# Kernel optimization log

Hardware: AMD Instinct MI355X
Metric: run time of the kernel (lower is better)

Reference implementation:

```python
import jax, jax.numpy as jnp
import numpy as np

N = 100000
E = 1600000
D_IN = 128
HID = 128
N_CLASSES = 40
NEG_SLOPE = 0.2  # PyG GATConv default
BN_EPS = 1e-5


def setup_inputs() -> dict:
    key = jax.random.key(0)
    ks = jax.random.split(key, 16)
    s = 0.1
    return {
        "x": jax.random.normal(ks[0], (N, D_IN), dtype=jnp.float32),
        "edge_index": jax.random.randint(ks[1], (2, E), 0, N, dtype=jnp.int64),
        # GAT layer 1 (in=D_IN, out=HID, heads=1)
        "W1": jax.random.normal(ks[2], (D_IN, HID), dtype=jnp.float32) * s,
        "a_src1": jax.random.normal(ks[3], (HID,), dtype=jnp.float32) * s,
        "a_dst1": jax.random.normal(ks[4], (HID,), dtype=jnp.float32) * s,
        "b1": jnp.zeros((HID,), dtype=jnp.float32),
        # GAT layer 2 (in=HID, out=HID, heads=1)
        "W2": jax.random.normal(ks[5], (HID, HID), dtype=jnp.float32) * s,
        "a_src2": jax.random.normal(ks[6], (HID,), dtype=jnp.float32) * s,
        "a_dst2": jax.random.normal(ks[7], (HID,), dtype=jnp.float32) * s,
        "b2": jnp.zeros((HID,), dtype=jnp.float32),
        # shared BatchNorm1d(HID) applied after every conv
        "gamma": jnp.ones((HID,), dtype=jnp.float32),
        "beta": jnp.zeros((HID,), dtype=jnp.float32),
        # output Linear(HID, N_CLASSES)
        "Wout": jax.random.normal(ks[8], (HID, N_CLASSES), dtype=jnp.float32) * s,
        "bout": jnp.zeros((N_CLASSES,), dtype=jnp.float32),
    }


def reference(x, edge_index, W1, a_src1, a_dst1, b1, W2, a_src2, a_dst2, b2,
              gamma, beta, Wout, bout):
    n = x.shape[0]
    loops = jnp.arange(n, dtype=edge_index.dtype)  # add_self_loops (GATConv default)
    src = jnp.concatenate([edge_index[0], loops])
    dst = jnp.concatenate([edge_index[1], loops])

    def gat_layer(h_in, W, a_s, a_d, b):
        h = h_in @ W                                   # [N, HID]
        e_src = h @ a_s                                # [N] per-node src score
        e_dst = h @ a_d                                # [N] per-node dst score
        e = jax.nn.leaky_relu(e_src[src] + e_dst[dst], NEG_SLOPE)  # [E+N]
        # segment softmax over incoming edges of each dst node
        m = jax.ops.segment_max(e, dst, num_segments=n)
        p = jnp.exp(e - m[dst])
        denom = jax.ops.segment_sum(p, dst, num_segments=n)
        alpha = p / denom[dst]
        out = jax.ops.segment_sum(alpha[:, None] * h[src], dst, num_segments=n)
        return out + b

    def bn_elu(z):
        mu = z.mean(axis=0)
        var = ((z - mu) ** 2).mean(axis=0)  # biased var (BN training mode)
        zh = (z - mu) / jnp.sqrt(var + BN_EPS) * gamma + beta
        return jax.nn.elu(zh)

    h = bn_elu(gat_layer(x, W1, a_src1, a_dst1, b1))
    h = bn_elu(gat_layer(h, W2, a_src2, a_dst2, b2))
    return h @ Wout + bout
```

## Files before the change

kernel.cpp:

```cpp
#include <hip/hip_runtime.h>

#define NNODES 100000
#define NEDGES 1600000
#define ET (NEDGES + NNODES)
#define NBUCK 782
#define NEG 0.2f
#define BNEPS 1e-5f
#define EPB 4096
#define NBLK_E ((ET + EPB - 1) / EPB)
#define CAP 4096

typedef __attribute__((ext_vector_type(8))) short short8;
typedef __attribute__((ext_vector_type(4))) float floatx4;
typedef __attribute__((ext_vector_type(2))) float floatx2;

__device__ __forceinline__ unsigned short f2b(float x) {
    unsigned int u = __float_as_uint(x);
    u += 0x7fff + ((u >> 16) & 1);
    return (unsigned short)(u >> 16);
}
__device__ __forceinline__ float b2f(unsigned short u) {
    return __uint_as_float(((unsigned int)u) << 16);
}
__device__ __forceinline__ float blo2f(unsigned int v) {
    return __uint_as_float(v << 16);
}
__device__ __forceinline__ float bhi2f(unsigned int v) {
    return __uint_as_float(v & 0xffff0000u);
}
__device__ __forceinline__ floatx2 u2f2(unsigned int v) {
    floatx2 r;
    r.x = __uint_as_float(v << 16);
    r.y = __uint_as_float(v & 0xffff0000u);
    return r;
}

__device__ __forceinline__ int edge_src(const int* ei, int e, int w64) {
    if (e >= NEDGES) return e - NEDGES;
    return w64 ? ei[2 * e] : ei[e];
}
__device__ __forceinline__ int edge_dst(const int* ei, int e, int w64) {
    if (e >= NEDGES) return e - NEDGES;
    return w64 ? ei[2 * (NEDGES + e)] : ei[NEDGES + e];
}

__global__ void k_prep(const float* __restrict__ W1, const float* __restrict__ W2,
                       unsigned short* __restrict__ WT1, unsigned short* __restrict__ WT2,
                       const int* ei, int* flag, int* bcur, float* bnstat) {
    int t = blockIdx.x * 256 + threadIdx.x;
    if (t < 800) bcur[t] = t * CAP;
    if (blockIdx.x == 4) {
        bnstat[threadIdx.x] = 0.f;
    } else if (blockIdx.x == 5) {
        bnstat[256 + threadIdx.x] = 0.f;
    }
    if (t == 1) {
        int is64 = 1;
        for (int j = 1; j < 16; j += 2)
            if (ei[j] != 0) is64 = 0;
        *flag = is64;
    }
    int k = t >> 7, n = t & 127;
    WT1[n * 128 + k] = f2b(W1[t]);
    WT2[n * 128 + k] = f2b(W2[t]);
}

__global__ __launch_bounds__(256) void k_bscatter(const int* __restrict__ ei,
                                                  const int* flag, int* bcur,
                                                  int* __restrict__ pairs) {
    __shared__ int lc[784];
    __shared__ int lbase[784];
    int t = threadIdx.x;
    for (int i = t; i < NBUCK; i += 256) lc[i] = 0;
    __syncthreads();
    int w64 = *flag;
    int base = blockIdx.x * EPB;
    for (int j = 0; j < EPB / 512; j++) {
        int e = base + j * 512 + t * 2;
        if (e + 1 < NEDGES) {
            int d0, d1;
            if (w64) {
                int4 dv = *(const int4*)&ei[2 * (NEDGES + e)];
                d0 = dv.x; d1 = dv.z;
            } else {
                int2 dv = *(const int2*)&ei[NEDGES + e];
                d0 = dv.x; d1 = dv.y;
            }
            atomicAdd(&lc[d0 >> 7], 1);
            atomicAdd(&lc[d1 >> 7], 1);
        } else {
            for (int k = 0; k < 2; k++) {
                int ee = e + k;
                if (ee < ET) atomicAdd(&lc[edge_dst(ei, ee, w64) >> 7], 1);
            }
        }
    }
    __syncthreads();
    for (int i = t; i < NBUCK; i += 256)
        if (lc[i]) lbase[i] = atomicAdd(&bcur[i], lc[i]);
    __syncthreads();
    for (int j = 0; j < EPB / 512; j++) {
        int e = base + j * 512 + t * 2;
        if (e + 1 < NEDGES) {
            int s0, s1, d0, d1;
            if (w64) {
                int4 sv = *(const int4*)&ei[2 * e];
                int4 dv = *(const int4*)&ei[2 * (NEDGES + e)];
                s0 = sv.x; s1 = sv.z; d0 = dv.x; d1 = dv.z;
            } else {
                int2 sv = *(const int2*)&ei[e];
                int2 dv = *(const int2*)&ei[NEDGES + e];
                s0 = sv.x; s1 = sv.y; d0 = dv.x; d1 = dv.y;
            }
            int p0 = atomicAdd(&lbase[d0 >> 7], 1);
            pairs[p0] = (s0 << 7) | (d0 & 127);
            int p1 = atomicAdd(&lbase[d1 >> 7], 1);
            pairs[p1] = (s1 << 7) | (d1 & 127);
        } else {
            for (int k = 0; k < 2; k++) {
                int ee = e + k;
                if (ee < ET) {
                    int src = edge_src(ei, ee, w64);
                    int dst = edge_dst(ei, ee, w64);
                    int pos = atomicAdd(&lbase[dst >> 7], 1);
                    pairs[pos] = (src << 7) | (dst & 127);
                }
            }
        }
    }
}

__global__ __launch_bounds__(256) void k_bsort(const int* __restrict__ pairs,
                                               const int* __restrict__ bcur,
                                               int2* __restrict__ rowse,
                                               int* __restrict__ srcs) {
    __shared__ int ncnt[128];
    __shared__ int nbase[128];
    __shared__ int sscan[128];
    int b = blockIdx.x, t = threadIdx.x;
    if (t < 128) ncnt[t] = 0;
    __syncthreads();
    int s0 = b * CAP, s1 = bcur[b];
    for (int i = s0 + t; i < s1; i += 256)
        atomicAdd(&ncnt[pairs[i] & 127], 1);
    __syncthreads();
    int v = (t < 128) ? ncnt[t] : 0;
    if (t < 128) sscan[t] = v;
    __syncthreads();
    for (int off = 1; off < 128; off <<= 1) {
        int add = (t < 128 && t >= off) ? sscan[t - off] : 0;
        __syncthreads();
        if (t < 128) sscan[t] += add;
        __syncthreads();
    }
    if (t < 128) {
        int excl = sscan[t] - v;
        nbase[t] = excl;
        int node = b * 128 + t;
        if (node < NNODES) rowse[node] = make_int2(s0 + excl, s0 + excl + v);
    }
    __syncthreads();
    if (t < 128) ncnt[t] = nbase[t];
    __syncthreads();
    for (int i = s0 + t; i < s1; i += 256) {
        int pr = pairs[i];
        int off = atomicAdd(&ncnt[pr & 127], 1);
        srcs[s0 + off] = ((unsigned int)pr) >> 7;
    }
}

template<bool BN>
__global__ __launch_bounds__(256) void k_gemm(const void* __restrict__ Ain,
        const unsigned short* __restrict__ WTg,
        const float* __restrict__ sums, const float* __restrict__ sqs,
        const float* __restrict__ gamma, const float* __restrict__ beta,
        const float* __restrict__ a_s, const float* __restrict__ a_d,
        float* __restrict__ es, float* __restrict__ ed,
        unsigned short* __restrict__ hB, int n) {
    __shared__ unsigned short lA[128][136];
    __shared__ unsigned short lW[128][136];
    __shared__ float las[128], lad[128];
    __shared__ float lsc[128], lsh[128];
    int t = threadIdx.x;
    int row0 = blockIdx.x * 128;
    if (t < 128) { las[t] = a_s[t]; lad[t] = a_d[t]; }
    if (BN && t < 128) {
        float mu = sums[t] * (1.f / NNODES);
        float var = fmaxf(sqs[t] * (1.f / NNODES) - mu * mu, 0.f);
        float s = gamma[t] * rsqrtf(var + BNEPS);
        lsc[t] = s;
        lsh[t] = beta[t] - mu * s;
    }

    const uint4* wt4 = (const uint4*)WTg;
#pragma unroll
    for (int j = 0; j < 8; j++) {
        int idx = t + j * 256;
        *(uint4*)&lW[idx >> 4][(idx & 15) * 8] = wt4[idx];
    }
    if (BN) __syncthreads();

    if (BN) {
        const uint4* Ab = (const uint4*)Ain;
#pragma unroll
        for (int j = 0; j < 8; j++) {
            int idx = t + j * 256;
            int r = idx >> 4, seg = idx & 15;
            uint4 v = make_uint4(0, 0, 0, 0);
            if (row0 + r < n) v = Ab[(size_t)(row0 + r) * 16 + seg];
            float f[8];
            f[0] = blo2f(v.x); f[1] = bhi2f(v.x);
            f[2] = blo2f(v.y); f[3] = bhi2f(v.y);
            f[4] = blo2f(v.z); f[5] = bhi2f(v.z);
            f[6] = blo2f(v.w); f[7] = bhi2f(v.w);
            unsigned short us[8];
#pragma unroll
            for (int k = 0; k < 8; k++) {
                int c = seg * 8 + k;
                float z = fmaf(f[k], lsc[c], lsh[c]);
                z = z > 0.f ? z : __expf(z) - 1.f;
                us[k] = f2b(z);
            }
            ushort4 u0, u1;
            u0.x = us[0]; u0.y = us[1]; u0.z = us[2]; u0.w = us[3];
            u1.x = us[4]; u1.y = us[5]; u1.z = us[6]; u1.w = us[7];
            *(ushort4*)&lA[r][seg * 8] = u0;
            *(ushort4*)&lA[r][seg * 8 + 4] = u1;
        }
    } else {
        const float* Af = (const float*)Ain;
#pragma unroll
        for (int j = 0; j < 16; j++) {
            int idx = t + j * 256;
            int r = idx >> 5, c4 = idx & 31;
            float4 v = make_float4(0.f, 0.f, 0.f, 0.f);
            if (row0 + r < n) v = ((const float4*)Af)[(size_t)(row0 + r) * 32 + c4];
            ushort4 u;
            u.x = f2b(v.x); u.y = f2b(v.y); u.z = f2b(v.z); u.w = f2b(v.w);
            *(ushort4*)&lA[r][c4 * 4] = u;
        }
    }
    __syncthreads();

    int w = t >> 6, lane = t & 63;
    int m = lane & 15, q = lane >> 4;
    int ar0 = w * 32 + m, ar1 = w * 32 + 16 + m;
    floatx4 acc0[8], acc1[8];
#pragma unroll
    for (int ct = 0; ct < 8; ct++) { acc0[ct] = (floatx4)0.0f; acc1[ct] = (floatx4)0.0f; }

#pragma unroll
    for (int kt = 0; kt < 4; kt++) {
        int kb = kt * 32 + q * 8;
        short8 af0 = *(const short8*)&lA[ar0][kb];
        short8 af1 = *(const short8*)&lA[ar1][kb];
#pragma unroll
        for (int ct = 0; ct < 8; ct++) {
            short8 bf = *(const short8*)&lW[ct * 16 + m][kb];
            acc0[ct] = __builtin_amdgcn_mfma_f32_16x16x32_bf16(af0, bf, acc0[ct], 0, 0, 0);
            acc1[ct] = __builtin_amdgcn_mfma_f32_16x16x32_bf16(af1, bf, acc1[ct], 0, 0, 0);
        }
    }

    __syncthreads();
#pragma unroll
    for (int ct = 0; ct < 8; ct++)
#pragma unroll
        for (int r = 0; r < 4; r++) {
            lA[w * 32 + q * 4 + r][ct * 16 + m] = f2b(acc0[ct][r]);
            lA[w * 32 + 16 + q * 4 + r][ct * 16 + m] = f2b(acc1[ct][r]);
        }
    __syncthreads();
#pragma unroll
    for (int j = 0; j < 8; j++) {
        int idx = t + j * 256;
        int r = idx >> 4, seg = idx & 15;
        int grow = row0 + r;
        if (grow < n) {
            uint4 v = *(const uint4*)&lA[r][seg * 8];
            ((uint4*)hB)[(size_t)grow * 16 + seg] = v;
        }
    }
    int r = t >> 1, q2 = t & 1;
    float s1 = 0.f, s2 = 0.f;
#pragma unroll
    for (int k = 0; k < 32; k++) {
        int c = q2 * 64 + 2 * k;
        unsigned int u = *(const unsigned int*)&lA[r][c];
        float va = blo2f(u), vb = bhi2f(u);
        s1 += va * las[c] + vb * las[c + 1];
        s2 += va * lad[c] + vb * lad[c + 1];
    }
    s1 += __shfl_xor(s1, 1, 64);
    s2 += __shfl_xor(s2, 1, 64);
    if (q2 == 0 && row0 + r < n) { es[row0 + r] = s1; ed[row0 + r] = s2; }
}

__global__ __launch_bounds__(256) void k_attn(const unsigned short* __restrict__ hB,
                                              const int* __restrict__ srcs,
                                              const int2* __restrict__ rowse,
                                              const float* __restrict__ es,
                                              const float* __restrict__ ed,
                                              const float* __restrict__ bias,
                                              unsigned short* __restrict__ haggB, int n) {
    __shared__ uint2 sp[8][32];
    int w = (blockIdx.x * 256 + threadIdx.x) >> 5;
    if (w >= n) return;
    int hw = threadIdx.x >> 5;
    int lane32 = threadIdx.x & 31;
    int g = lane32 >> 4, l16 = lane32 & 15;
    int2 se = rowse[w];
    int start = se.x, end = se.y;
    float edv = ed[w];
    const uint4* hp4 = (const uint4*)hB;
    floatx2 a0 = {0.f, 0.f}, a1 = {0.f, 0.f}, a2 = {0.f, 0.f}, a3 = {0.f, 0.f};
    float den = 0.f;

    for (int chunk = start; chunk < end; chunk += 32) {
        int i = chunk + lane32;
        int sv = 0; float pv = 0.f;
        if (i < end) {
            sv = srcs[i];
            float e = es[sv] + edv;
            e = e > 0.f ? e : NEG * e;
            pv = __expf(e);
            den += pv;
        }
        sp[hw][lane32] = make_uint2((unsigned)sv, __float_as_uint(pv));
        int cnt = min(32, end - chunk);
        for (int j = 0; j < cnt; j += 8) {
            uint2 e0 = sp[hw][j + g];
            uint2 e1 = sp[hw][j + 2 + g];
            uint2 e2 = sp[hw][j + 4 + g];
            uint2 e3 = sp[hw][j + 6 + g];
            uint4 h0 = hp4[e0.x * 16u + l16];
            uint4 h1 = hp4[e1.x * 16u + l16];
            uint4 h2 = hp4[e2.x * 16u + l16];
            uint4 h3 = hp4[e3.x * 16u + l16];
            float p0 = __uint_as_float(e0.y), p1 = __uint_as_float(e1.y);
            float p2 = __uint_as_float(e2.y), p3 = __uint_as_float(e3.y);
            floatx2 P0 = {p0, p0};
            a0 += P0 * u2f2(h0.x); a1 += P0 * u2f2(h0.y);
            a2 += P0 * u2f2(h0.z); a3 += P0 * u2f2(h0.w);
            floatx2 P1 = {p1, p1};
            a0 += P1 * u2f2(h1.x); a1 += P1 * u2f2(h1.y);
            a2 += P1 * u2f2(h1.z); a3 += P1 * u2f2(h1.w);
            floatx2 P2 = {p2, p2};
            a0 += P2 * u2f2(h2.x); a1 += P2 * u2f2(h2.y);
            a2 += P2 * u2f2(h2.z); a3 += P2 * u2f2(h2.w);
            floatx2 P3 = {p3, p3};
            a0 += P3 * u2f2(h3.x); a1 += P3 * u2f2(h3.y);
            a2 += P3 * u2f2(h3.z); a3 += P3 * u2f2(h3.w);
        }
    }
    den += __shfl_xor(den, 1, 64);  den += __shfl_xor(den, 2, 64);
    den += __shfl_xor(den, 4, 64);  den += __shfl_xor(den, 8, 64);
    den += __shfl_xor(den, 16, 64);
    a0.x += __shfl_xor(a0.x, 16, 64); a0.y += __shfl_xor(a0.y, 16, 64);
    a1.x += __shfl_xor(a1.x, 16, 64); a1.y += __shfl_xor(a1.y, 16, 64);
    a2.x += __shfl_xor(a2.x, 16, 64); a2.y += __shfl_xor(a2.y, 16, 64);
    a3.x += __shfl_xor(a3.x, 16, 64); a3.y += __shfl_xor(a3.y, 16, 64);
    if (g == 0) {
        float inv = 1.f / den;
        const float2* b2p = (const float2*)bias;
        float2 c0 = b2p[l16 * 4 + 0], c1 = b2p[l16 * 4 + 1];
        float2 c2 = b2p[l16 * 4 + 2], c3 = b2p[l16 * 4 + 3];
        uint4 o;
        o.x = (unsigned int)f2b(fmaf(a0.x, inv, c0.x)) |
              ((unsigned int)f2b(fmaf(a0.y, inv, c0.y)) << 16);
        o.y = (unsigned int)f2b(fmaf(a1.x, inv, c1.x)) |
              ((unsigned int)f2b(fmaf(a1.y, inv, c1.y)) << 16);
        o.z = (unsigned int)f2b(fmaf(a2.x, inv, c2.x)) |
              ((unsigned int)f2b(fmaf(a2.y, inv, c2.y)) << 16);
        o.w = (unsigned int)f2b(fmaf(a3.x, inv, c3.x)) |
              ((unsigned int)f2b(fmaf(a3.y, inv, c3.y)) << 16);
        ((uint4*)haggB)[(size_t)w * 16 + l16] = o;
    }
}

__global__ __launch_bounds__(256) void k_bnstats(const unsigned short* __restrict__ hin,
                                                 float* sums, float* sqs, int n) {
    __shared__ float red[4][256];
    int t = threadIdx.x;
    int c2 = t & 63, quarter = t >> 6;
    int r0 = blockIdx.x * 256;
    int rend = min(r0 + 256, n);
    const unsigned int* hp = (const unsigned int*)hin;
    float s0 = 0.f, q0 = 0.f, s1 = 0.f, q1 = 0.f;
    for (int r = r0 + quarter; r < rend; r += 4) {
        unsigned int v = hp[(size_t)r * 64 + c2];
        float a = blo2f(v), b = bhi2f(v);
        s0 += a; q0 += a * a;
        s1 += b; q1 += b * b;
    }
    *(float4*)&red[quarter][c2 * 4] = make_float4(s0, q0, s1, q1);
    __syncthreads();
    float v = red[0][t] + red[1][t] + red[2][t] + red[3][t];
    int c2i = t >> 2, k = t & 3;
    int ch = c2i * 2 + (k >> 1);
    if (k & 1) atomicAdd(&sqs[ch], v);
    else       atomicAdd(&sums[ch], v);
}

__global__ __launch_bounds__(256) void k_outgemm(const unsigned short* __restrict__ h,
                                                 const float* __restrict__ sums,
                                                 const float* __restrict__ sqs,
                                                 const float* __restrict__ gamma,
                                                 const float* __restrict__ beta,
                                                 const float* __restrict__ Wout,
                                                 const float* __restrict__ bout,
                                                 float* __restrict__ out, int n) {
    __shared__ float lsc[128], lsh[128];
    __shared__ float lacc[2][64][41];
    int t = threadIdx.x;
    if (t < 128) {
        float mu = sums[t] * (1.f / NNODES);
        float var = fmaxf(sqs[t] * (1.f / NNODES) - mu * mu, 0.f);
        float s = gamma[t] * rsqrtf(var + BNEPS);
        lsc[t] = s;
        lsh[t] = beta[t] - mu * s;
    }
    __syncthreads();
    int wv = __builtin_amdgcn_readfirstlane(t >> 6);
    int lane = t & 63;
    int pairId = wv >> 1, jq = wv & 1;
    int row = blockIdx.x * 128 + pairId * 64 + lane;
    bool valid = row < n;
    const uint4* hb4 = (const uint4*)h;
    uint4 hreg[8];
#pragma unroll
    for (int s8 = 0; s8 < 8; s8++) {
        hreg[s8] = make_uint4(0, 0, 0, 0);
        if (valid) hreg[s8] = hb4[(size_t)row * 16 + jq * 8 + s8];
    }
    const float* wbase = Wout + jq * 64 * 40;
    float acc[40];
#pragma unroll
    for (int j = 0; j < 40; j++) acc[j] = 0.f;
#pragma unroll
    for (int k8 = 0; k8 < 8; k8++) {
        uint4 v = hreg[k8];
        float f[8];
        f[0] = blo2f(v.x); f[1] = bhi2f(v.x);
        f[2] = blo2f(v.y); f[3] = bhi2f(v.y);
        f[4] = blo2f(v.z); f[5] = bhi2f(v.z);
        f[6] = blo2f(v.w); f[7] = bhi2f(v.w);
#pragma unroll
        for (int kk = 0; kk < 8; kk++) {
            int c = jq * 64 + k8 * 8 + kk;
            float z = fmaf(f[kk], lsc[c], lsh[c]);
            z = z > 0.f ? z : __expf(z) - 1.f;
            const float4* wr = (const float4*)(wbase + (k8 * 8 + kk) * 40);
#pragma unroll
            for (int j4 = 0; j4 < 10; j4++) {
                float4 wv4 = wr[j4];
                acc[j4 * 4 + 0] = fmaf(z, wv4.x, acc[j4 * 4 + 0]);
                acc[j4 * 4 + 1] = fmaf(z, wv4.y, acc[j4 * 4 + 1]);
                acc[j4 * 4 + 2] = fmaf(z, wv4.z, acc[j4 * 4 + 2]);
                acc[j4 * 4 + 3] = fmaf(z, wv4.w, acc[j4 * 4 + 3]);
            }
        }
    }
    if (jq == 1) {
#pragma unroll
        for (int j = 0; j < 40; j++) lacc[pairId][lane][j] = acc[j];
    }
    __syncthreads();
    if (jq == 0 && valid) {
        const float4* b4 = (const float4*)bout;
        float4* outp = (float4*)(out + (size_t)row * 40);
#pragma unroll
        for (int j4 = 0; j4 < 10; j4++) {
            float4 bv = b4[j4];
            float4 o;
            o.x = acc[j4 * 4 + 0] + lacc[pairId][lane][j4 * 4 + 0] + bv.x;
            o.y = acc[j4 * 4 + 1] + lacc[pairId][lane][j4 * 4 + 1] + bv.y;
            o.z = acc[j4 * 4 + 2] + lacc[pairId][lane][j4 * 4 + 2] + bv.z;
            o.w = acc[j4 * 4 + 3] + lacc[pairId][lane][j4 * 4 + 3] + bv.w;
            outp[j4] = o;
        }
    }
}

extern "C" void kernel_launch(void* const* d_in, const int* in_sizes, int n_in,
                              void* d_out, int out_size, void* d_ws, size_t ws_size,
                              hipStream_t stream) {
    const float* x      = (const float*)d_in[0];
    const int*   ei     = (const int*)d_in[1];
    const float* W1     = (const float*)d_in[2];
    const float* a_src1 = (const float*)d_in[3];
    const float* a_dst1 = (const float*)d_in[4];
    const float* b1     = (const float*)d_in[5];
    const float* W2     = (const float*)d_in[6];
    const float* a_src2 = (const float*)d_in[7];
    const float* a_dst2 = (const float*)d_in[8];
    const float* b2     = (const float*)d_in[9];
    const float* gamma  = (const float*)d_in[10];
    const float* beta   = (const float*)d_in[11];
    const float* Wout   = (const float*)d_in[12];
    const float* bout   = (const float*)d_in[13];
    float* out = (float*)d_out;

    char* p = (char*)d_ws;
    auto alloc = [&](size_t bytes) -> void* {
        void* r = (void*)p;
        p += (bytes + 255) & ~(size_t)255;
        return r;
    };
    unsigned short* hB    = (unsigned short*)alloc((size_t)NNODES * 128 * 2);
    unsigned short* haggB = (unsigned short*)alloc((size_t)NNODES * 128 * 2);
    float* es     = (float*)alloc((size_t)NNODES * 4);
    float* ed     = (float*)alloc((size_t)NNODES * 4);
    int*   pairs  = (int*)alloc((size_t)NBUCK * CAP * 4);
    int*   srcs   = (int*)alloc((size_t)NBUCK * CAP * 4);
    int2*  rowse  = (int2*)alloc((size_t)NNODES * 8);
    int*   bcur   = (int*)alloc(800 * 4);
    float* bnstat = (float*)alloc(4 * 128 * 4);
    unsigned short* WT1 = (unsigned short*)alloc(128 * 128 * 2);
    unsigned short* WT2 = (unsigned short*)alloc(128 * 128 * 2);
    int*   flag   = (int*)alloc(4);

    float* sum1 = bnstat, *sq1 = bnstat + 128, *sum2 = bnstat + 256, *sq2 = bnstat + 384;

    k_prep<<<64, 256, 0, stream>>>(W1, W2, WT1, WT2, ei, flag, bcur, bnstat);
    k_bscatter<<<NBLK_E, 256, 0, stream>>>(ei, flag, bcur, pairs);
    k_bsort<<<NBUCK, 256, 0, stream>>>(pairs, bcur, rowse, srcs);

    const int GB = (NNODES + 127) / 128;
    const int AB = NNODES / 8;
    const int SB = (NNODES + 255) / 256;
    const int OB = (NNODES + 127) / 128;

    k_gemm<false><<<GB, 256, 0, stream>>>(x, WT1, nullptr, nullptr, nullptr, nullptr,
                                          a_src1, a_dst1, es, ed, hB, NNODES);
    k_attn<<<AB, 256, 0, stream>>>(hB, srcs, rowse, es, ed, b1, haggB, NNODES);
    k_bnstats<<<SB, 256, 0, stream>>>(haggB, sum1, sq1, NNODES);

    k_gemm<true><<<GB, 256, 0, stream>>>(haggB, WT2, sum1, sq1, gamma, beta,
                                         a_src2, a_dst2, es, ed, hB, NNODES);
    k_attn<<<AB, 256, 0, stream>>>(hB, srcs, rowse, es, ed, b2, haggB, NNODES);
    k_bnstats<<<SB, 256, 0, stream>>>(haggB, sum2, sq2, NNODES);

    k_outgemm<<<OB, 256, 0, stream>>>(haggB, sum2, sq2, gamma, beta, Wout, bout, out, NNODES);

    (void)in_sizes; (void)n_in; (void)out_size; (void)ws_size;
}
```

Measured before the change: 402.9 us.

## Fuse BN statistics into attention kernel and use MFMA split-bf16 output GEMM

Folds the batch-norm sum and sum-of-squares reduction into the attention aggregation kernel through shared-memory atomics and 16 slotted global partials, which removes two k_bnstats launches and the extra pass over haggB. The output linear layer becomes a bf16 MFMA GEMM. Activations and Wout are each split into high and low bf16 halves to keep accuracy close to fp32, and results are staged through LDS so the stores are coalesced. The cost is many LDS atomics per node in attention, global atomic contention on the slots, and three MFMAs per tile in place of one.

```diff
diff --git a/kernel.cpp b/kernel.cpp
--- a/kernel.cpp
+++ b/kernel.cpp
@@ -9,6 +9,7 @@
 #define EPB 4096
 #define NBLK_E ((ET + EPB - 1) / EPB)
 #define CAP 4096
+#define NSLOT 16
 
 typedef __attribute__((ext_vector_type(8))) short short8;
 typedef __attribute__((ext_vector_type(4))) float floatx4;
@@ -45,20 +46,25 @@
 }
 
 __global__ void k_prep(const float* __restrict__ W1, const float* __restrict__ W2,
+                       const float* __restrict__ Wout,
                        unsigned short* __restrict__ WT1, unsigned short* __restrict__ WT2,
-                       const int* ei, int* flag, int* bcur, float* bnstat) {
+                       unsigned short* __restrict__ WoT1, unsigned short* __restrict__ WoT2,
+                       const int* ei, int* flag, int* bcur, float* gpart) {
     int t = blockIdx.x * 256 + threadIdx.x;
     if (t < 800) bcur[t] = t * CAP;
-    if (blockIdx.x == 4) {
-        bnstat[threadIdx.x] = 0.f;
-    } else if (blockIdx.x == 5) {
-        bnstat[256 + threadIdx.x] = 0.f;
-    }
+    if (t < 2 * NSLOT * 256) gpart[t] = 0.f;
     if (t == 1) {
         int is64 = 1;
         for (int j = 1; j < 16; j += 2)
             if (ei[j] != 0) is64 = 0;
         *flag = is64;
+    }
+    if (t < 6144) {
+        int j = t >> 7, k = t & 127;
+        float wv = (j < 40) ? Wout[k * 40 + j] : 0.f;
+        unsigned short w1 = f2b(wv);
+        WoT1[t] = w1;
+        WoT2[t] = f2b(wv - b2f(w1));
     }
     int k = t >> 7, n = t & 127;
     WT1[n * 128 + k] = f2b(W1[t]);
@@ -172,7 +178,7 @@
 template<bool BN>
 __global__ __launch_bounds__(256) void k_gemm(const void* __restrict__ Ain,
         const unsigned short* __restrict__ WTg,
-        const float* __restrict__ sums, const float* __restrict__ sqs,
+        const float* __restrict__ gpart,
         const float* __restrict__ gamma, const float* __restrict__ beta,
         const float* __restrict__ a_s, const float* __restrict__ a_d,
         float* __restrict__ es, float* __restrict__ ed,
@@ -185,11 +191,17 @@
     int row0 = blockIdx.x * 128;
     if (t < 128) { las[t] = a_s[t]; lad[t] = a_d[t]; }
     if (BN && t < 128) {
-        float mu = sums[t] * (1.f / NNODES);
-        float var = fmaxf(sqs[t] * (1.f / NNODES) - mu * mu, 0.f);
-        float s = gamma[t] * rsqrtf(var + BNEPS);
-        lsc[t] = s;
-        lsh[t] = beta[t] - mu * s;
+        float s = 0.f, q = 0.f;
+#pragma unroll
+        for (int si = 0; si < NSLOT; si++) {
+            s += gpart[si * 256 + t];
+            q += gpart[si * 256 + 128 + t];
+        }
+        float mu = s * (1.f / NNODES);
+        float var = fmaxf(q * (1.f / NNODES) - mu * mu, 0.f);
+        float sc = gamma[t] * rsqrtf(var + BNEPS);
+        lsc[t] = sc;
+        lsh[t] = beta[t] - mu * sc;
     }
 
     const uint4* wt4 = (const uint4*)WTg;
@@ -302,16 +314,25 @@
                                               const float* __restrict__ es,
                                               const float* __restrict__ ed,
                                               const float* __restrict__ bias,
-                                              unsigned short* __restrict__ haggB, int n) {
+                                              unsigned short* __restrict__ haggB,
+                                              float* __restrict__ gpart, int n) {
     __shared__ uint2 sp[8][32];
-    int w = (blockIdx.x * 256 + threadIdx.x) >> 5;
-    if (w >= n) return;
-    int hw = threadIdx.x >> 5;
-    int lane32 = threadIdx.x & 31;
+    __shared__ float bsum[128], bsqs[128];
+    int t = threadIdx.x;
+    if (t < 128) { bsum[t] = 0.f; bsqs[t] = 0.f; }
+    __syncthreads();
+    int w = (blockIdx.x * 256 + t) >> 5;
+    bool active = (w < n);
+    int hw = t >> 5;
+    int lane32 = t & 31;
     int g = lane32 >> 4, l16 = lane32 & 15;
-    int2 se = rowse[w];
-    int start = se.x, end = se.y;
-    float edv = ed[w];
+    int start = 0, end = 0;
+    float edv = 0.f;
+    if (active) {
+        int2 se = rowse[w];
+        start = se.x; end = se.y;
+        edv = ed[w];
+    }
     const uint4* hp4 = (const uint4*)hB;
     floatx2 a0 = {0.f, 0.f}, a1 = {0.f, 0.f}, a2 = {0.f, 0.f}, a3 = {0.f, 0.f};
     float den = 0.f;
@@ -360,7 +381,7 @@
     a1.x += __shfl_xor(a1.x, 16, 64); a1.y += __shfl_xor(a1.y, 16, 64);
     a2.x += __shfl_xor(a2.x, 16, 64); a2.y += __shfl_xor(a2.y, 16, 64);
     a3.x += __shfl_xor(a3.x, 16, 64); a3.y += __shfl_xor(a3.y, 16, 64);
-    if (g == 0) {
+    if (g == 0 && active) {
         float inv = 1.f / den;
         const float2* b2p = (const float2*)bias;
         float2 c0 = b2p[l16 * 4 + 0], c1 = b2p[l16 * 4 + 1];
@@ -375,111 +396,133 @@
         o.w = (unsigned int)f2b(fmaf(a3.x, inv, c3.x)) |
               ((unsigned int)f2b(fmaf(a3.y, inv, c3.y)) << 16);
         ((uint4*)haggB)[(size_t)w * 16 + l16] = o;
-    }
-}
-
-__global__ __launch_bounds__(256) void k_bnstats(const unsigned short* __restrict__ hin,
-                                                 float* sums, float* sqs, int n) {
-    __shared__ float red[4][256];
-    int t = threadIdx.x;
-    int c2 = t & 63, quarter = t >> 6;
-    int r0 = blockIdx.x * 256;
-    int rend = min(r0 + 256, n);
-    const unsigned int* hp = (const unsigned int*)hin;
-    float s0 = 0.f, q0 = 0.f, s1 = 0.f, q1 = 0.f;
-    for (int r = r0 + quarter; r < rend; r += 4) {
-        unsigned int v = hp[(size_t)r * 64 + c2];
-        float a = blo2f(v), b = bhi2f(v);
-        s0 += a; q0 += a * a;
-        s1 += b; q1 += b * b;
-    }
-    *(float4*)&red[quarter][c2 * 4] = make_float4(s0, q0, s1, q1);
-    __syncthreads();
-    float v = red[0][t] + red[1][t] + red[2][t] + red[3][t];
-    int c2i = t >> 2, k = t & 3;
-    int ch = c2i * 2 + (k >> 1);
-    if (k & 1) atomicAdd(&sqs[ch], v);
-    else       atomicAdd(&sums[ch], v);
+        int cb = l16 * 8;
+        float v0 = blo2f(o.x), v1 = bhi2f(o.x);
+        float v2 = blo2f(o.y), v3 = bhi2f(o.y);
+        float v4 = blo2f(o.z), v5 = bhi2f(o.z);
+        float v6 = blo2f(o.w), v7 = bhi2f(o.w);
+        atomicAdd(&bsum[cb + 0], v0); atomicAdd(&bsqs[cb + 0], v0 * v0);
+        atomicAdd(&bsum[cb + 1], v1); atomicAdd(&bsqs[cb + 1], v1 * v1);
+        atomicAdd(&bsum[cb + 2], v2); atomicAdd(&bsqs[cb + 2], v2 * v2);
+        atomicAdd(&bsum[cb + 3], v3); atomicAdd(&bsqs[cb + 3], v3 * v3);
+        atomicAdd(&bsum[cb + 4], v4); atomicAdd(&bsqs[cb + 4], v4 * v4);
+        atomicAdd(&bsum[cb + 5], v5); atomicAdd(&bsqs[cb + 5], v5 * v5);
+        atomicAdd(&bsum[cb + 6], v6); atomicAdd(&bsqs[cb + 6], v6 * v6);
+        atomicAdd(&bsum[cb + 7], v7); atomicAdd(&bsqs[cb + 7], v7 * v7);
+    }
+    __syncthreads();
+    int slot = (blockIdx.x & (NSLOT - 1)) * 256;
+    if (t < 128) atomicAdd(&gpart[slot + t], bsum[t]);
+    else         atomicAdd(&gpart[slot + t], bsqs[t - 128]);
 }
 
 __global__ __launch_bounds__(256) void k_outgemm(const unsigned short* __restrict__ h,
-                                                 const float* __restrict__ sums,
-                                                 const float* __restrict__ sqs,
+                                                 const float* __restrict__ gpart,
                                                  const float* __restrict__ gamma,
                                                  const float* __restrict__ beta,
-                                                 const float* __restrict__ Wout,
+                                                 const unsigned short* __restrict__ WoT1,
+                                                 const unsigned short* __restrict__ WoT2,
                                                  const float* __restrict__ bout,
                                                  float* __restrict__ out, int n) {
+    __shared__ unsigned short lA1[128][136];
+    __shared__ unsigned short lA2[128][136];
     __shared__ float lsc[128], lsh[128];
-    __shared__ float lacc[2][64][41];
+    __shared__ float lb[48];
     int t = threadIdx.x;
     if (t < 128) {
-        float mu = sums[t] * (1.f / NNODES);
-        float var = fmaxf(sqs[t] * (1.f / NNODES) - mu * mu, 0.f);
-        float s = gamma[t] * rsqrtf(var + BNEPS);
-        lsc[t] = s;
-        lsh[t] = beta[t] - mu * s;
-    }
-    __syncthreads();
-    int wv = __builtin_amdgcn_readfirstlane(t >> 6);
-    int lane = t & 63;
-    int pairId = wv >> 1, jq = wv & 1;
-    int row = blockIdx.x * 128 + pairId * 64 + lane;
-    bool valid = row < n;
-    const uint4* hb4 = (const uint4*)h;
-    uint4 hreg[8];
-#pragma unroll
-    for (int s8 = 0; s8 < 8; s8++) {
-        hreg[s8] = make_uint4(0, 0, 0, 0);
-        if (valid) hreg[s8] = hb4[(size_t)row * 16 + jq * 8 + s8];
-    }
-    const float* wbase = Wout + jq * 64 * 40;
-    float acc[40];
-#pragma unroll
-    for (int j = 0; j < 40; j++) acc[j] = 0.f;
-#pragma unroll
-    for (int k8 = 0; k8 < 8; k8++) {
-        uint4 v = hreg[k8];
+        float s = 0.f, q = 0.f;
+#pragma unroll
+        for (int si = 0; si < NSLOT; si++) {
+            s += gpart[si * 256 + t];
+            q += gpart[si * 256 + 128 + t];
+        }
+        float mu = s * (1.f / NNODES);
+        float var = fmaxf(q * (1.f / NNODES) - mu * mu, 0.f);
+        float sc = gamma[t] * rsqrtf(var + BNEPS);
+        lsc[t] = sc;
+        lsh[t] = beta[t] - mu * sc;
+    }
+    if (t >= 128 && t < 176) lb[t - 128] = (t < 168) ? bout[t - 128] : 0.f;
+    __syncthreads();
+    int row0 = blockIdx.x * 128;
+    const uint4* Ab = (const uint4*)h;
+#pragma unroll
+    for (int j = 0; j < 8; j++) {
+        int idx = t + j * 256;
+        int r = idx >> 4, seg = idx & 15;
+        uint4 v = make_uint4(0, 0, 0, 0);
+        if (row0 + r < n) v = Ab[(size_t)(row0 + r) * 16 + seg];
         float f[8];
         f[0] = blo2f(v.x); f[1] = bhi2f(v.x);
         f[2] = blo2f(v.y); f[3] = bhi2f(v.y);
         f[4] = blo2f(v.z); f[5] = bhi2f(v.z);
         f[6] = blo2f(v.w); f[7] = bhi2f(v.w);
-#pragma unroll
-        for (int kk = 0; kk < 8; kk++) {
-            int c = jq * 64 + k8 * 8 + kk;
-            float z = fmaf(f[kk], lsc[c], lsh[c]);
+        unsigned short u1[8], u2[8];
+#pragma unroll
+        for (int k = 0; k < 8; k++) {
+            int c = seg * 8 + k;
+            float z = fmaf(f[k], lsc[c], lsh[c]);
             z = z > 0.f ? z : __expf(z) - 1.f;
-            const float4* wr = (const float4*)(wbase + (k8 * 8 + kk) * 40);
-#pragma unroll
-            for (int j4 = 0; j4 < 10; j4++) {
-                float4 wv4 = wr[j4];
-                acc[j4 * 4 + 0] = fmaf(z, wv4.x, acc[j4 * 4 + 0]);
-                acc[j4 * 4 + 1] = fmaf(z, wv4.y, acc[j4 * 4 + 1]);
-                acc[j4 * 4 + 2] = fmaf(z, wv4.z, acc[j4 * 4 + 2]);
-                acc[j4 * 4 + 3] = fmaf(z, wv4.w, acc[j4 * 4 + 3]);
+            unsigned short b1 = f2b(z);
+            u1[k] = b1;
+            u2[k] = f2b(z - b2f(b1));
+        }
+        ushort4 a, b;
+        a.x = u1[0]; a.y = u1[1]; a.z = u1[2]; a.w = u1[3];
+        b.x = u1[4]; b.y = u1[5]; b.z = u1[6]; b.w = u1[7];
+        *(ushort4*)&lA1[r][seg * 8] = a;
+        *(ushort4*)&lA1[r][seg * 8 + 4] = b;
+        a.x = u2[0]; a.y = u2[1]; a.z = u2[2]; a.w = u2[3];
+        b.x = u2[4]; b.y = u2[5]; b.z = u2[6]; b.w = u2[7];
+        *(ushort4*)&lA2[r][seg * 8] = a;
+        *(ushort4*)&lA2[r][seg * 8 + 4] = b;
+    }
+    __syncthreads();
+
+    int w = t >> 6, lane = t & 63;
+    int m = lane & 15, q4 = lane >> 4;
+    floatx4 acc0[3], acc1[3];
+#pragma unroll
+    for (int ct = 0; ct < 3; ct++) { acc0[ct] = (floatx4)0.0f; acc1[ct] = (floatx4)0.0f; }
+#pragma unroll
+    for (int kt = 0; kt < 4; kt++) {
+        int kb = kt * 32 + q4 * 8;
+        short8 a10 = *(const short8*)&lA1[w * 32 + m][kb];
+        short8 a11 = *(const short8*)&lA1[w * 32 + 16 + m][kb];
+        short8 a20 = *(const short8*)&lA2[w * 32 + m][kb];
+        short8 a21 = *(const short8*)&lA2[w * 32 + 16 + m][kb];
+#pragma unroll
+        for (int ct = 0; ct < 3; ct++) {
+            short8 bf1 = *(const short8*)&WoT1[(ct * 16 + m) * 128 + kb];
+            short8 bf2 = *(const short8*)&WoT2[(ct * 16 + m) * 128 + kb];
+            acc0[ct] = __builtin_amdgcn_mfma_f32_16x16x32_bf16(a10, bf1, acc0[ct], 0, 0, 0);
+            acc0[ct] = __builtin_amdgcn_mfma_f32_16x16x32_bf16(a20, bf1, acc0[ct], 0, 0, 0);
+            acc0[ct] = __builtin_amdgcn_mfma_f32_16x16x32_bf16(a10, bf2, acc0[ct], 0, 0, 0);
+            acc1[ct] = __builtin_amdgcn_mfma_f32_16x16x32_bf16(a11, bf1, acc1[ct], 0, 0, 0);
+            acc1[ct] = __builtin_amdgcn_mfma_f32_16x16x32_bf16(a21, bf1, acc1[ct], 0, 0, 0);
+            acc1[ct] = __builtin_amdgcn_mfma_f32_16x16x32_bf16(a11, bf2, acc1[ct], 0, 0, 0);
+        }
+    }
+    __syncthreads();
+    float* stage = (float*)&lA1[0][0];
+#pragma unroll
+    for (int ct = 0; ct < 3; ct++) {
+        int col = ct * 16 + m;
+        if (col < 40) {
+            float bb = lb[col];
+#pragma unroll
+            for (int r = 0; r < 4; r++) {
+                stage[(w * 32 + q4 * 4 + r) * 40 + col] = acc0[ct][r] + bb;
+                stage[(w * 32 + 16 + q4 * 4 + r) * 40 + col] = acc1[ct][r] + bb;
             }
         }
     }
-    if (jq == 1) {
-#pragma unroll
-        for (int j = 0; j < 40; j++) lacc[pairId][lane][j] = acc[j];
-    }
-    __syncthreads();
-    if (jq == 0 && valid) {
-        const float4* b4 = (const float4*)bout;
-        float4* outp = (float4*)(out + (size_t)row * 40);
-#pragma unroll
-        for (int j4 = 0; j4 < 10; j4++) {
-            float4 bv = b4[j4];
-            float4 o;
-            o.x = acc[j4 * 4 + 0] + lacc[pairId][lane][j4 * 4 + 0] + bv.x;
-            o.y = acc[j4 * 4 + 1] + lacc[pairId][lane][j4 * 4 + 1] + bv.y;
-            o.z = acc[j4 * 4 + 2] + lacc[pairId][lane][j4 * 4 + 2] + bv.z;
-            o.w = acc[j4 * 4 + 3] + lacc[pairId][lane][j4 * 4 + 3] + bv.w;
-            outp[j4] = o;
-        }
-    }
+    __syncthreads();
+    int rowsLeft = n - row0; if (rowsLeft > 128) rowsLeft = 128;
+    int nf4 = rowsLeft * 10;
+    const float4* st4 = (const float4*)stage;
+    float4* outp = (float4*)(out + (size_t)row0 * 40);
+    for (int i = t; i < nf4; i += 256) outp[i] = st4[i];
 }
 
 extern "C" void kernel_launch(void* const* d_in, const int* in_sizes, int n_in,
@@ -515,33 +558,35 @@
     int*   srcs   = (int*)alloc((size_t)NBUCK * CAP * 4);
     int2*  rowse  = (int2*)alloc((size_t)NNODES * 8);
     int*   bcur   = (int*)alloc(800 * 4);
-    float* bnstat = (float*)alloc(4 * 128 * 4);
-    unsigned short* WT1 = (unsigned short*)alloc(128 * 128 * 2);
-    unsigned short* WT2 = (unsigned short*)alloc(128 * 128 * 2);
+    float* gpart  = (float*)alloc(2 * NSLOT * 256 * 4);
+    unsigned short* WT1  = (unsigned short*)alloc(128 * 128 * 2);
+    unsigned short* WT2  = (unsigned short*)alloc(128 * 128 * 2);
+    unsigned short* WoT1 = (unsigned short*)alloc(48 * 128 * 2);
+    unsigned short* WoT2 = (unsigned short*)alloc(48 * 128 * 2);
     int*   flag   = (int*)alloc(4);
 
-    float* sum1 = bnstat, *sq1 = bnstat + 128, *sum2 = bnstat + 256, *sq2 = bnstat + 384;
-
-    k_prep<<<64, 256, 0, stream>>>(W1, W2, WT1, WT2, ei, flag, bcur, bnstat);
+    float* part1 = gpart;
+    float* part2 = gpart + NSLOT * 256;
+
+    k_prep<<<64, 256, 0, stream>>>(W1, W2, Wout, WT1, WT2, WoT1, WoT2,
+                                   ei, flag, bcur, gpart);
     k_bscatter<<<NBLK_E, 256, 0, stream>>>(ei, flag, bcur, pairs);
     k_bsort<<<NBUCK, 256, 0, stream>>>(pairs, bcur, rowse, srcs);
 
     const int GB = (NNODES + 127) / 128;
     const int AB = NNODES / 8;
-    const int SB = (NNODES + 255) / 256;
     const int OB = (NNODES + 127) / 128;
 
-    k_gemm<false><<<GB, 256, 0, stream>>>(x, WT1, nullptr, nullptr, nullptr, nullptr,
+    k_gemm<false><<<GB, 256, 0, stream>>>(x, WT1, nullptr, nullptr, nullptr,
                                           a_src1, a_dst1, es, ed, hB, NNODES);
-    k_attn<<<AB, 256, 0, stream>>>(hB, srcs, rowse, es, ed, b1, haggB, NNODES);
-    k_bnstats<<<SB, 256, 0, stream>>>(haggB, sum1, sq1, NNODES);
-
-    k_gemm<true><<<GB, 256, 0, stream>>>(haggB, WT2, sum1, sq1, gamma, beta,
+    k_attn<<<AB, 256, 0, stream>>>(hB, srcs, rowse, es, ed, b1, haggB, part1, NNODES);
+
+    k_gemm<true><<<GB, 256, 0, stream>>>(haggB, WT2, part1, gamma, beta,
                                          a_src2, a_dst2, es, ed, hB, NNODES);
-    k_attn<<<AB, 256, 0, stream>>>(hB, srcs, rowse, es, ed, b2, haggB, NNODES);
-    k_bnstats<<<SB, 256, 0, stream>>>(haggB, sum2, sq2, NNODES);
-
-    k_outgemm<<<OB, 256, 0, stream>>>(haggB, sum2, sq2, gamma, beta, Wout, bout, out, NNODES);
+    k_attn<<<AB, 256, 0, stream>>>(hB, srcs, rowse, es, ed, b2, haggB, part2, NNODES);
+
+    k_outgemm<<<OB, 256, 0, stream>>>(haggB, part2, gamma, beta, WoT1, WoT2,
+                                      bout, out, NNODES);
 
     (void)in_sizes; (void)n_in; (void)out_size; (void)ws_size;
 }
```

After: 524.1 us. +30.1%, slower.
